# Kernel tuning notes

Hardware: AMD Instinct MI355X
Metric: run time of the kernel (lower is better)

Reference implementation:

```python
import jax, jax.numpy as jnp
import numpy as np

SEQ, D_IN, D_OUT = 8192, 1024, 1024


def setup_inputs() -> dict:
    key = jax.random.key(0)
    kx, kq, kk, kv = jax.random.split(key, 4)
    # torch nn.Linear weights have shape (out_features, in_features)
    s = 1.0 / np.sqrt(D_IN)
    return {
        "x": jax.random.normal(kx, (SEQ, D_IN), dtype=jnp.float32),
        "Wq": jax.random.uniform(kq, (D_OUT, D_IN), dtype=jnp.float32, minval=-s, maxval=s),
        "Wk": jax.random.uniform(kk, (D_OUT, D_IN), dtype=jnp.float32, minval=-s, maxval=s),
        "Wv": jax.random.uniform(kv, (D_OUT, D_IN), dtype=jnp.float32, minval=-s, maxval=s),
    }


def reference(x, Wq, Wk, Wv):
    # Linear (no bias): y = x @ W.T
    q = x @ Wq.T          # [S, D_OUT]
    k = x @ Wk.T          # [S, D_OUT]
    v = x @ Wv.T          # [S, D_OUT]
    scale = 1.0 / jnp.sqrt(jnp.asarray(k.shape[-1], dtype=x.dtype))
    scores = (q @ k.T) * scale            # [S, S]
    weights = jax.nn.softmax(scores, axis=-1)
    return weights @ v                    # [S, D_OUT]
```

## Files before the change

### kernel.cpp

```cpp
#include <hip/hip_runtime.h>
#include <hip/hip_bf16.h>
#include <stdint.h>


#define SEQ 8192
#define DMODEL 1024
#define LOG2E 1.44269504088896340736f
#define GROUP_M 8

typedef __bf16 bf16_t;
typedef __bf16 bf16x8 __attribute__((ext_vector_type(8)));
typedef float f32x4 __attribute__((ext_vector_type(4)));

__global__ __launch_bounds__(256)
void convert_f32_bf16(const float* __restrict__ in, bf16_t* __restrict__ out, long n) {
    long i = ((long)blockIdx.x * 256 + threadIdx.x) * 4;
    if (i + 3 < n) {
        const float4 v = *(const float4*)(in + i);
        union { ushort4 u; bf16_t b[4]; } p;
        p.b[0] = (bf16_t)v.x; p.b[1] = (bf16_t)v.y;
        p.b[2] = (bf16_t)v.z; p.b[3] = (bf16_t)v.w;
        *(ushort4*)(out + i) = p.u;
    }
}

__global__ __launch_bounds__(256)
void add_f32(float* __restrict__ out, const float* __restrict__ part, long n) {
    long i = ((long)blockIdx.x * 256 + threadIdx.x) * 4;
    if (i + 3 < n) {
        float4 a = *(const float4*)(out + i);
        const float4 b = *(const float4*)(part + i);
        a.x += b.x; a.y += b.y; a.z += b.z; a.w += b.w;
        *(float4*)(out + i) = a;
    }
}

__global__ __launch_bounds__(256)
void zero_f32(float* __restrict__ p, int n) {
    int i = blockIdx.x * 256 + threadIdx.x;
    if (i < n) p[i] = 0.0f;
}

template <typename OutT, int MODE>
__global__ __launch_bounds__(512, 2)
void gemm_nt(const bf16_t* __restrict__ A, const bf16_t* __restrict__ B,
             OutT* __restrict__ C0, OutT* __restrict__ C1,
             float* __restrict__ lsum,
             int M, int N, int Kps, int lda, int ldb, int ldc,
             long plane, int cshift, float alpha)
{
    __shared__ bf16_t As[2][256 * 64];
    __shared__ bf16_t Bs[2][256 * 64];

    const int tid  = threadIdx.x;
    const int wave = tid >> 6;
    const int lane = tid & 63;

    const int nbm = M >> 8, nbn = N >> 8;
    const int tiles = nbm * nbn;
    int bid = blockIdx.x;
    const int sid = bid / tiles;
    bid -= sid * tiles;
    const long kbase = (long)sid * Kps;
    OutT* __restrict__ C = sid ? C1 : C0;

    const int per_group = GROUP_M * nbn;
    const int gid   = bid / per_group;
    const int rem   = bid - gid * per_group;
    const int first = gid * GROUP_M;
    const int gsz   = min(nbm - first, GROUP_M);
    const int bm    = first + rem % gsz;
    const int bn    = rem / gsz;
    const long row0 = (long)bm * 256;
    const long col0 = (long)bn * 256;

    const int wm = (wave >> 2) * 128;
    const int wn = (wave & 3) * 64;
    const int lr = lane & 15;
    const int lq = lane >> 4;

    const int rt = tid >> 3;
    const int sl = ((tid & 7) + rt) & 7;
    const bf16_t* pa = A + (row0 + rt) * (long)lda + kbase + sl * 8;
    const bf16_t* pb = B + (col0 + rt) * (long)ldb + kbase + sl * 8;

    const int p0  = (lq - lr) & 7;
    const int p1  = p0 ^ 4;
    const int oA0 = (wm + lr) * 64 + p0 * 8;
    const int oA1 = (wm + lr) * 64 + p1 * 8;
    const int oB0 = (wn + lr) * 64 + p0 * 8;
    const int oB1 = (wn + lr) * 64 + p1 * 8;

    const int nt = Kps >> 6;

    f32x4 acc[8][4] = {};

#define STG_A(kt, bsel, i0)                                                     \
    {                                                                           \
        _Pragma("unroll")                                                       \
        for (int ii = 0; ii < 2; ++ii) {                                        \
            const int i = (i0) + ii;                                            \
            const bf16_t* ga = pa + (long)(kt) * 64 + (long)i * 64 * lda;       \
            __builtin_amdgcn_global_load_lds(                                   \
                (const __attribute__((address_space(1))) uint32_t*)ga,          \
                (__attribute__((address_space(3))) uint32_t*)(As[bsel] + i * 4096 + tid * 8), \
                16, 0, 0);                                                      \
        }                                                                       \
    }
#define STG_B(kt, bsel, i0)                                                     \
    {                                                                           \
        _Pragma("unroll")                                                       \
        for (int ii = 0; ii < 2; ++ii) {                                        \
            const int i = (i0) + ii;                                            \
            const bf16_t* gb = pb + (long)(kt) * 64 + (long)i * 64 * ldb;       \
            __builtin_amdgcn_global_load_lds(                                   \
                (const __attribute__((address_space(1))) uint32_t*)gb,          \
                (__attribute__((address_space(3))) uint32_t*)(Bs[bsel] + i * 4096 + tid * 8), \
                16, 0, 0);                                                      \
        }                                                                       \
    }

    STG_A(0, 0, 0); STG_A(0, 0, 2); STG_B(0, 0, 0); STG_B(0, 0, 2);
    if (nt > 1) STG_A(1, 1, 0);
    asm volatile("s_waitcnt vmcnt(2)" ::: "memory");
    __builtin_amdgcn_s_barrier();

    for (int t = 0; t < nt; ++t) {
        const int c = t & 1;
        const bf16_t* as = As[c];
        const bf16_t* bs = Bs[c];
        const int s1 = (t + 1 < nt);
        const int s2 = (t + 2 < nt);

        bf16x8 a0k0[4], a0k1[4], a1k0[4], a1k1[4];
        bf16x8 b0k0[2], b0k1[2], b1k0[2], b1k1[2];

        #pragma unroll
        for (int mi = 0; mi < 4; ++mi) {
            a0k0[mi] = *(const bf16x8*)(as + oA0 + mi * 1024);
            a0k1[mi] = *(const bf16x8*)(as + oA1 + mi * 1024);
        }
        #pragma unroll
        for (int ni = 0; ni < 2; ++ni) {
            b0k0[ni] = *(const bf16x8*)(bs + oB0 + ni * 1024);
            b0k1[ni] = *(const bf16x8*)(bs + oB1 + ni * 1024);
        }
        if (s1) STG_A(t + 1, c ^ 1, 2);
        asm volatile("s_waitcnt lgkmcnt(8)" ::: "memory");
        __builtin_amdgcn_s_barrier();
        asm volatile("s_waitcnt lgkmcnt(0)" ::: "memory");
        __builtin_amdgcn_s_setprio(1);
        #pragma unroll
        for (int mi = 0; mi < 4; ++mi)
            #pragma unroll
            for (int ni = 0; ni < 2; ++ni)
                acc[mi][ni] = __builtin_amdgcn_mfma_f32_16x16x32_bf16(
                    a0k0[mi], b0k0[ni], acc[mi][ni], 0, 0, 0);
        #pragma unroll
        for (int mi = 0; mi < 4; ++mi)
            #pragma unroll
            for (int ni = 0; ni < 2; ++ni)
                acc[mi][ni] = __builtin_amdgcn_mfma_f32_16x16x32_bf16(
                    a0k1[mi], b0k1[ni], acc[mi][ni], 0, 0, 0);
        __builtin_amdgcn_s_setprio(0);
        __builtin_amdgcn_s_barrier();

        #pragma unroll
        for (int ni = 0; ni < 2; ++ni) {
            b1k0[ni] = *(const bf16x8*)(bs + oB0 + (ni + 2) * 1024);
            b1k1[ni] = *(const bf16x8*)(bs + oB1 + (ni + 2) * 1024);
        }
        if (s1) STG_B(t + 1, c ^ 1, 0);
        __builtin_amdgcn_s_barrier();
        asm volatile("s_waitcnt lgkmcnt(0)" ::: "memory");
        __builtin_amdgcn_s_setprio(1);
        #pragma unroll
        for (int mi = 0; mi < 4; ++mi)
            #pragma unroll
            for (int ni = 0; ni < 2; ++ni)
                acc[mi][ni + 2] = __builtin_amdgcn_mfma_f32_16x16x32_bf16(
                    a0k0[mi], b1k0[ni], acc[mi][ni + 2], 0, 0, 0);
        #pragma unroll
        for (int mi = 0; mi < 4; ++mi)
            #pragma unroll
            for (int ni = 0; ni < 2; ++ni)
                acc[mi][ni + 2] = __builtin_amdgcn_mfma_f32_16x16x32_bf16(
                    a0k1[mi], b1k1[ni], acc[mi][ni + 2], 0, 0, 0);
        __builtin_amdgcn_s_setprio(0);
        __builtin_amdgcn_s_barrier();

        #pragma unroll
        for (int mi = 0; mi < 4; ++mi) {
            a1k0[mi] = *(const bf16x8*)(as + oA0 + (mi + 4) * 1024);
            a1k1[mi] = *(const bf16x8*)(as + oA1 + (mi + 4) * 1024);
        }
        if (s1) STG_B(t + 1, c ^ 1, 2);
        __builtin_amdgcn_s_barrier();
        asm volatile("s_waitcnt lgkmcnt(0)" ::: "memory");
        __builtin_amdgcn_s_setprio(1);
        #pragma unroll
        for (int mi = 0; mi < 4; ++mi)
            #pragma unroll
            for (int ni = 0; ni < 2; ++ni)
                acc[mi + 4][ni] = __builtin_amdgcn_mfma_f32_16x16x32_bf16(
                    a1k0[mi], b0k0[ni], acc[mi + 4][ni], 0, 0, 0);
        #pragma unroll
        for (int mi = 0; mi < 4; ++mi)
            #pragma unroll
            for (int ni = 0; ni < 2; ++ni)
                acc[mi + 4][ni] = __builtin_amdgcn_mfma_f32_16x16x32_bf16(
                    a1k1[mi], b0k1[ni], acc[mi + 4][ni], 0, 0, 0);
        __builtin_amdgcn_s_setprio(0);
        __builtin_amdgcn_s_barrier();

        if (s2) STG_A(t + 2, c, 0);
        asm volatile("s_waitcnt vmcnt(2)" ::: "memory");
        __builtin_amdgcn_s_barrier();
        __builtin_amdgcn_s_setprio(1);
        #pragma unroll
        for (int mi = 0; mi < 4; ++mi)
            #pragma unroll
            for (int ni = 0; ni < 2; ++ni)
                acc[mi + 4][ni + 2] = __builtin_amdgcn_mfma_f32_16x16x32_bf16(
                    a1k0[mi], b1k0[ni], acc[mi + 4][ni + 2], 0, 0, 0);
        #pragma unroll
        for (int mi = 0; mi < 4; ++mi)
            #pragma unroll
            for (int ni = 0; ni < 2; ++ni)
                acc[mi + 4][ni + 2] = __builtin_amdgcn_mfma_f32_16x16x32_bf16(
                    a1k1[mi], b1k1[ni], acc[mi + 4][ni + 2], 0, 0, 0);
        __builtin_amdgcn_s_setprio(0);
        __builtin_amdgcn_s_barrier();
    }
#undef STG_A
#undef STG_B

    OutT* __restrict__ Cb = C + (col0 >> cshift) * plane;
    const int ccol0 = (int)(col0 & (((long)1 << cshift) - 1));

    if (MODE == 1) {
        #pragma unroll
        for (int mi = 0; mi < 8; ++mi)
            #pragma unroll
            for (int rg = 0; rg < 4; ++rg) {
                const long r = row0 + wm + mi * 16 + lq * 4 + rg;
                float part = 0.f;
                #pragma unroll
                for (int ni = 0; ni < 4; ++ni) {
                    const int c = ccol0 + wn + ni * 16 + lr;
                    const float e = exp2f(alpha * acc[mi][ni][rg]);
                    part += e;
                    Cb[r * (long)ldc + c] = (OutT)e;
                }
                part += __shfl_xor(part, 1);
                part += __shfl_xor(part, 2);
                part += __shfl_xor(part, 4);
                part += __shfl_xor(part, 8);
                if (lr == 0) atomicAdd(&lsum[r], part);
            }
    } else if (MODE == 2) {
        #pragma unroll
        for (int mi = 0; mi < 8; ++mi)
            #pragma unroll
            for (int rg = 0; rg < 4; ++rg) {
                const long r = row0 + wm + mi * 16 + lq * 4 + rg;
                const float inv = 1.0f / lsum[r];
                #pragma unroll
                for (int ni = 0; ni < 4; ++ni) {
                    const int c = ccol0 + wn + ni * 16 + lr;
                    Cb[r * (long)ldc + c] = (OutT)(acc[mi][ni][rg] * inv);
                }
            }
    } else {
        #pragma unroll
        for (int mi = 0; mi < 8; ++mi)
            #pragma unroll
            for (int ni = 0; ni < 4; ++ni)
                #pragma unroll
                for (int rg = 0; rg < 4; ++rg) {
                    const long r = row0 + wm + mi * 16 + lq * 4 + rg;
                    const int  c = ccol0 + wn + ni * 16 + lr;
                    Cb[r * (long)ldc + c] = (OutT)(alpha * acc[mi][ni][rg]);
                }
    }
}

__global__ __launch_bounds__(256)
void transpose_bf16(const bf16_t* __restrict__ in, bf16_t* __restrict__ out,
                    int R, int ldin, int ldout)
{
    __shared__ bf16_t tile[32][33];
    const int tx = threadIdx.x & 31;
    const int ty = threadIdx.x >> 5;
    const int c0 = blockIdx.x * 32;
    const int r0 = blockIdx.y * 32;
    #pragma unroll
    for (int j = 0; j < 32; j += 8)
        tile[ty + j][tx] = in[(long)(r0 + ty + j) * ldin + c0 + tx];
    __syncthreads();
    #pragma unroll
    for (int j = 0; j < 32; j += 8)
        out[(long)(c0 + ty + j) * ldout + r0 + tx] = tile[tx][ty + j];
}

extern "C" void kernel_launch(void* const* d_in, const int* in_sizes, int n_in,
                              void* d_out, int out_size, void* d_ws, size_t ws_size,
                              hipStream_t stream)
{
    const float* x  = (const float*)d_in[0];
    const float* Wq = (const float*)d_in[1];
    const float* Wk = (const float*)d_in[2];
    const float* Wv = (const float*)d_in[3];
    float* out = (float*)d_out;

    char* ws = (char*)d_ws;
    const long XN = (long)SEQ * DMODEL;
    const long WN = (long)DMODEL * DMODEL;
    const long SN = (long)SEQ * SEQ;

    bf16_t* xb   = (bf16_t*)ws;
    bf16_t* wcat = (bf16_t*)(ws + XN * 2);
    bf16_t* qb   = (bf16_t*)(ws + XN * 2 + WN * 6);
    bf16_t* kb   = qb + XN;
    bf16_t* vb   = qb + 2 * XN;
    bf16_t* Sb   = (bf16_t*)(ws + XN * 2 + WN * 6 + XN * 6);
    float*  pvp  = (float*)(ws + XN * 2 + WN * 6 + XN * 6 + SN * 2);
    float*  lsum = (float*)(ws + XN * 2 + WN * 6 + XN * 6 + SN * 2 + XN * 4);
    bf16_t* vtb  = xb;

    const size_t base_need = (size_t)(XN * 2 + WN * 6 + XN * 6 + SN * 2);
    const bool use_split = ws_size >= base_need + XN * 4 + SEQ * 4;
    if (!use_split) lsum = (float*)(ws + base_need);

    convert_f32_bf16<<<(int)(XN / 4 / 256), 256, 0, stream>>>(x,  xb, XN);
    convert_f32_bf16<<<(int)(WN / 4 / 256), 256, 0, stream>>>(Wq, wcat,          WN);
    convert_f32_bf16<<<(int)(WN / 4 / 256), 256, 0, stream>>>(Wk, wcat + WN,     WN);
    convert_f32_bf16<<<(int)(WN / 4 / 256), 256, 0, stream>>>(Wv, wcat + 2 * WN, WN);
    zero_f32<<<SEQ / 256, 256, 0, stream>>>(lsum, SEQ);

    dim3 blk256(256);
    dim3 blk512(512);
    gemm_nt<bf16_t, 0><<<(SEQ / 256) * (3 * DMODEL / 256), blk512, 0, stream>>>(
        xb, wcat, qb, qb, nullptr, SEQ, 3 * DMODEL, DMODEL,
        DMODEL, DMODEL, DMODEL, XN, 10, 1.0f);

    transpose_bf16<<<dim3(DMODEL / 32, SEQ / 32), blk256, 0, stream>>>(
        vb, vtb, SEQ, DMODEL, SEQ);

    gemm_nt<bf16_t, 1><<<(SEQ / 256) * (SEQ / 256), blk512, 0, stream>>>(
        qb, kb, Sb, Sb, lsum, SEQ, SEQ, DMODEL,
        DMODEL, DMODEL, SEQ, 0, 30, 0.03125f * LOG2E);

    if (use_split) {
        gemm_nt<float, 2><<<2 * (SEQ / 256) * (DMODEL / 256), blk512, 0, stream>>>(
            Sb, vtb, out, pvp, lsum, SEQ, DMODEL, SEQ / 2,
            SEQ, SEQ, DMODEL, 0, 30, 1.0f);
        add_f32<<<(int)(XN / 4 / 256), 256, 0, stream>>>(out, pvp, XN);
    } else {
        gemm_nt<float, 2><<<(SEQ / 256) * (DMODEL / 256), blk512, 0, stream>>>(
            Sb, vtb, out, out, lsum, SEQ, DMODEL, SEQ,
            SEQ, SEQ, DMODEL, 0, 30, 1.0f);
    }
}
```

Measured before the change: 482.8 us.

## Software-pipeline LDS fragment loads across iterations and cut per-iteration barriers

Restructures the GEMM main loop so the first A/B register fragments for the next K-tile are read from LDS during the current tile's MFMA phases, instead of at the start of each iteration. It also drops most of the per-phase s_barriers in favour of sched_barrier and finer lgkmcnt waits, keeping a single workgroup barrier per iteration around the global-to-LDS staging. The aim is to hide LDS read latency behind MFMAs and reduce synchronisation stalls. In exchange it raises register pressure, and the looser barrier scheme risks LDS races on buffers that are still being overwritten.

Measured after the change: 528.2 us. 9.4% more time.

```diff
diff --git a/kernel.cpp b/kernel.cpp
--- a/kernel.cpp
+++ b/kernel.cpp
@@ -121,34 +121,46 @@
     }
 
     STG_A(0, 0, 0); STG_A(0, 0, 2); STG_B(0, 0, 0); STG_B(0, 0, 2);
-    if (nt > 1) STG_A(1, 1, 0);
-    asm volatile("s_waitcnt vmcnt(2)" ::: "memory");
+    if (nt > 1) {
+        STG_A(1, 1, 0);
+        asm volatile("s_waitcnt vmcnt(2)" ::: "memory");
+    } else {
+        asm volatile("s_waitcnt vmcnt(0)" ::: "memory");
+    }
     __builtin_amdgcn_s_barrier();
+
+    bf16x8 a0k0[4], a0k1[4], a1k0[4], a1k1[4];
+    bf16x8 b0k0[2], b0k1[2], b1k0[2], b1k1[2];
+
+    #pragma unroll
+    for (int mi = 0; mi < 4; ++mi) {
+        a0k0[mi] = *(const bf16x8*)(As[0] + oA0 + mi * 1024);
+        a0k1[mi] = *(const bf16x8*)(As[0] + oA1 + mi * 1024);
+    }
+    #pragma unroll
+    for (int ni = 0; ni < 2; ++ni) {
+        b0k0[ni] = *(const bf16x8*)(Bs[0] + oB0 + ni * 1024);
+        b0k1[ni] = *(const bf16x8*)(Bs[0] + oB1 + ni * 1024);
+    }
 
     for (int t = 0; t < nt; ++t) {
         const int c = t & 1;
-        const bf16_t* as = As[c];
-        const bf16_t* bs = Bs[c];
+        const bf16_t* as  = As[c];
+        const bf16_t* bs  = Bs[c];
+        const bf16_t* asn = As[c ^ 1];
+        const bf16_t* bsn = Bs[c ^ 1];
         const int s1 = (t + 1 < nt);
         const int s2 = (t + 2 < nt);
 
-        bf16x8 a0k0[4], a0k1[4], a1k0[4], a1k1[4];
-        bf16x8 b0k0[2], b0k1[2], b1k0[2], b1k1[2];
-
-        #pragma unroll
-        for (int mi = 0; mi < 4; ++mi) {
-            a0k0[mi] = *(const bf16x8*)(as + oA0 + mi * 1024);
-            a0k1[mi] = *(const bf16x8*)(as + oA1 + mi * 1024);
-        }
+        if (s1) { STG_A(t + 1, c ^ 1, 2); STG_B(t + 1, c ^ 1, 0); }
         #pragma unroll
         for (int ni = 0; ni < 2; ++ni) {
-            b0k0[ni] = *(const bf16x8*)(bs + oB0 + ni * 1024);
-            b0k1[ni] = *(const bf16x8*)(bs + oB1 + ni * 1024);
-        }
-        if (s1) STG_A(t + 1, c ^ 1, 2);
-        asm volatile("s_waitcnt lgkmcnt(8)" ::: "memory");
-        __builtin_amdgcn_s_barrier();
-        asm volatile("s_waitcnt lgkmcnt(0)" ::: "memory");
+            b1k0[ni] = *(const bf16x8*)(bs + oB0 + (ni + 2) * 1024);
+            b1k1[ni] = *(const bf16x8*)(bs + oB1 + (ni + 2) * 1024);
+        }
+
+        asm volatile("s_waitcnt lgkmcnt(4)" ::: "memory");
+        __builtin_amdgcn_sched_barrier(0);
         __builtin_amdgcn_s_setprio(1);
         #pragma unroll
         for (int mi = 0; mi < 4; ++mi)
@@ -163,16 +175,17 @@
                 acc[mi][ni] = __builtin_amdgcn_mfma_f32_16x16x32_bf16(
                     a0k1[mi], b0k1[ni], acc[mi][ni], 0, 0, 0);
         __builtin_amdgcn_s_setprio(0);
-        __builtin_amdgcn_s_barrier();
-
-        #pragma unroll
-        for (int ni = 0; ni < 2; ++ni) {
-            b1k0[ni] = *(const bf16x8*)(bs + oB0 + (ni + 2) * 1024);
-            b1k1[ni] = *(const bf16x8*)(bs + oB1 + (ni + 2) * 1024);
-        }
-        if (s1) STG_B(t + 1, c ^ 1, 0);
-        __builtin_amdgcn_s_barrier();
-        asm volatile("s_waitcnt lgkmcnt(0)" ::: "memory");
+        __builtin_amdgcn_sched_barrier(0);
+
+        #pragma unroll
+        for (int mi = 0; mi < 4; ++mi) {
+            a1k0[mi] = *(const bf16x8*)(as + oA0 + (mi + 4) * 1024);
+            a1k1[mi] = *(const bf16x8*)(as + oA1 + (mi + 4) * 1024);
+        }
+        if (s1) STG_B(t + 1, c ^ 1, 2);
+
+        asm volatile("s_waitcnt lgkmcnt(8)" ::: "memory");
+        __builtin_amdgcn_sched_barrier(0);
         __builtin_amdgcn_s_setprio(1);
         #pragma unroll
         for (int mi = 0; mi < 4; ++mi)
@@ -187,16 +200,27 @@
                 acc[mi][ni + 2] = __builtin_amdgcn_mfma_f32_16x16x32_bf16(
                     a0k1[mi], b1k1[ni], acc[mi][ni + 2], 0, 0, 0);
         __builtin_amdgcn_s_setprio(0);
+        __builtin_amdgcn_sched_barrier(0);
+
+        asm volatile("s_waitcnt lgkmcnt(0)" ::: "memory");
         __builtin_amdgcn_s_barrier();
-
-        #pragma unroll
-        for (int mi = 0; mi < 4; ++mi) {
-            a1k0[mi] = *(const bf16x8*)(as + oA0 + (mi + 4) * 1024);
-            a1k1[mi] = *(const bf16x8*)(as + oA1 + (mi + 4) * 1024);
-        }
-        if (s1) STG_B(t + 1, c ^ 1, 2);
+        if (s2) {
+            STG_A(t + 2, c, 0);
+            asm volatile("s_waitcnt vmcnt(2)" ::: "memory");
+        } else {
+            asm volatile("s_waitcnt vmcnt(0)" ::: "memory");
+        }
         __builtin_amdgcn_s_barrier();
-        asm volatile("s_waitcnt lgkmcnt(0)" ::: "memory");
+
+        if (s1) {
+            #pragma unroll
+            for (int mi = 0; mi < 4; ++mi) {
+                a0k0[mi] = *(const bf16x8*)(asn + oA0 + mi * 1024);
+                a0k1[mi] = *(const bf16x8*)(asn + oA1 + mi * 1024);
+            }
+        }
+        __builtin_amdgcn_sched_barrier(0);
+
         __builtin_amdgcn_s_setprio(1);
         #pragma unroll
         for (int mi = 0; mi < 4; ++mi)
@@ -211,11 +235,17 @@
                 acc[mi + 4][ni] = __builtin_amdgcn_mfma_f32_16x16x32_bf16(
                     a1k1[mi], b0k1[ni], acc[mi + 4][ni], 0, 0, 0);
         __builtin_amdgcn_s_setprio(0);
-        __builtin_amdgcn_s_barrier();
-
-        if (s2) STG_A(t + 2, c, 0);
-        asm volatile("s_waitcnt vmcnt(2)" ::: "memory");
-        __builtin_amdgcn_s_barrier();
+        __builtin_amdgcn_sched_barrier(0);
+
+        if (s1) {
+            #pragma unroll
+            for (int ni = 0; ni < 2; ++ni) {
+                b0k0[ni] = *(const bf16x8*)(bsn + oB0 + ni * 1024);
+                b0k1[ni] = *(const bf16x8*)(bsn + oB1 + ni * 1024);
+            }
+        }
+        __builtin_amdgcn_sched_barrier(0);
+
         __builtin_amdgcn_s_setprio(1);
         #pragma unroll
         for (int mi = 0; mi < 4; ++mi)
@@ -230,7 +260,7 @@
                 acc[mi + 4][ni + 2] = __builtin_amdgcn_mfma_f32_16x16x32_bf16(
                     a1k1[mi], b1k1[ni], acc[mi + 4][ni + 2], 0, 0, 0);
         __builtin_amdgcn_s_setprio(0);
-        __builtin_amdgcn_s_barrier();
+        __builtin_amdgcn_sched_barrier(0);
     }
 #undef STG_A
 #undef STG_B
@@ -247,10 +277,10 @@
                 float part = 0.f;
                 #pragma unroll
                 for (int ni = 0; ni < 4; ++ni) {
-                    const int c = ccol0 + wn + ni * 16 + lr;
+                    const int cc = ccol0 + wn + ni * 16 + lr;
                     const float e = exp2f(alpha * acc[mi][ni][rg]);
                     part += e;
-                    Cb[r * (long)ldc + c] = (OutT)e;
+                    Cb[r * (long)ldc + cc] = (OutT)e;
                 }
                 part += __shfl_xor(part, 1);
                 part += __shfl_xor(part, 2);
@@ -267,8 +297,8 @@
                 const float inv = 1.0f / lsum[r];
                 #pragma unroll
                 for (int ni = 0; ni < 4; ++ni) {
-                    const int c = ccol0 + wn + ni * 16 + lr;
-                    Cb[r * (long)ldc + c] = (OutT)(acc[mi][ni][rg] * inv);
+                    const int cc = ccol0 + wn + ni * 16 + lr;
+                    Cb[r * (long)ldc + cc] = (OutT)(acc[mi][ni][rg] * inv);
                 }
             }
     } else {
@@ -279,8 +309,8 @@
                 #pragma unroll
                 for (int rg = 0; rg < 4; ++rg) {
                     const long r = row0 + wm + mi * 16 + lq * 4 + rg;
-                    const int  c = ccol0 + wn + ni * 16 + lr;
-                    Cb[r * (long)ldc + c] = (OutT)(alpha * acc[mi][ni][rg]);
+                    const int  cc = ccol0 + wn + ni * 16 + lr;
+                    Cb[r * (long)ldc + cc] = (OutT)(alpha * acc[mi][ni][rg]);
                 }
     }
 }
```

## Replace interleaved partial-stage GEMM pipeline with simple double buffering

Applied to the files above, without the earlier changes.

Replaces the fine-grained schedule with plain double buffering in the GEMM main loop. The old loop split each tile's global-to-LDS loads into quarters spread across four MFMA phases, with several barriers per iteration and a stage two tiles ahead. Now each iteration waits for all loads, issues one barrier, then issues the whole next-tile prefetch before the LDS reads and MFMAs. This cuts barrier and waitcnt overhead per K-step, but the load issue is less interleaved with compute and the wait is coarser.

Measured after the change: 512.0 us. 6.0% more time.

```diff
diff --git a/kernel.cpp b/kernel.cpp
--- a/kernel.cpp
+++ b/kernel.cpp
@@ -95,23 +95,18 @@
 
     f32x4 acc[8][4] = {};
 
-#define STG_A(kt, bsel, i0)                                                     \
+#define STG8(kt, bsel)                                                          \
     {                                                                           \
         _Pragma("unroll")                                                       \
-        for (int ii = 0; ii < 2; ++ii) {                                        \
-            const int i = (i0) + ii;                                            \
+        for (int i = 0; i < 4; ++i) {                                           \
             const bf16_t* ga = pa + (long)(kt) * 64 + (long)i * 64 * lda;       \
             __builtin_amdgcn_global_load_lds(                                   \
                 (const __attribute__((address_space(1))) uint32_t*)ga,          \
                 (__attribute__((address_space(3))) uint32_t*)(As[bsel] + i * 4096 + tid * 8), \
                 16, 0, 0);                                                      \
         }                                                                       \
-    }
-#define STG_B(kt, bsel, i0)                                                     \
-    {                                                                           \
         _Pragma("unroll")                                                       \
-        for (int ii = 0; ii < 2; ++ii) {                                        \
-            const int i = (i0) + ii;                                            \
+        for (int i = 0; i < 4; ++i) {                                           \
             const bf16_t* gb = pb + (long)(kt) * 64 + (long)i * 64 * ldb;       \
             __builtin_amdgcn_global_load_lds(                                   \
                 (const __attribute__((address_space(1))) uint32_t*)gb,          \
@@ -120,21 +115,20 @@
         }                                                                       \
     }
 
-    STG_A(0, 0, 0); STG_A(0, 0, 2); STG_B(0, 0, 0); STG_B(0, 0, 2);
-    if (nt > 1) STG_A(1, 1, 0);
-    asm volatile("s_waitcnt vmcnt(2)" ::: "memory");
-    __builtin_amdgcn_s_barrier();
+    STG8(0, 0);
 
     for (int t = 0; t < nt; ++t) {
         const int c = t & 1;
         const bf16_t* as = As[c];
         const bf16_t* bs = Bs[c];
-        const int s1 = (t + 1 < nt);
-        const int s2 = (t + 2 < nt);
-
-        bf16x8 a0k0[4], a0k1[4], a1k0[4], a1k1[4];
-        bf16x8 b0k0[2], b0k1[2], b1k0[2], b1k1[2];
-
+
+        asm volatile("s_waitcnt vmcnt(0)" ::: "memory");
+        __builtin_amdgcn_s_barrier();
+        asm volatile("" ::: "memory");
+
+        if (t + 1 < nt) STG8(t + 1, c ^ 1);
+
+        bf16x8 a0k0[4], a0k1[4], b0k0[2], b0k1[2], b1k0[2], b1k1[2];
         #pragma unroll
         for (int mi = 0; mi < 4; ++mi) {
             a0k0[mi] = *(const bf16x8*)(as + oA0 + mi * 1024);
@@ -144,36 +138,24 @@
         for (int ni = 0; ni < 2; ++ni) {
             b0k0[ni] = *(const bf16x8*)(bs + oB0 + ni * 1024);
             b0k1[ni] = *(const bf16x8*)(bs + oB1 + ni * 1024);
-        }
-        if (s1) STG_A(t + 1, c ^ 1, 2);
-        asm volatile("s_waitcnt lgkmcnt(8)" ::: "memory");
-        __builtin_amdgcn_s_barrier();
-        asm volatile("s_waitcnt lgkmcnt(0)" ::: "memory");
-        __builtin_amdgcn_s_setprio(1);
-        #pragma unroll
-        for (int mi = 0; mi < 4; ++mi)
-            #pragma unroll
-            for (int ni = 0; ni < 2; ++ni)
-                acc[mi][ni] = __builtin_amdgcn_mfma_f32_16x16x32_bf16(
-                    a0k0[mi], b0k0[ni], acc[mi][ni], 0, 0, 0);
-        #pragma unroll
-        for (int mi = 0; mi < 4; ++mi)
-            #pragma unroll
-            for (int ni = 0; ni < 2; ++ni)
-                acc[mi][ni] = __builtin_amdgcn_mfma_f32_16x16x32_bf16(
-                    a0k1[mi], b0k1[ni], acc[mi][ni], 0, 0, 0);
-        __builtin_amdgcn_s_setprio(0);
-        __builtin_amdgcn_s_barrier();
-
-        #pragma unroll
-        for (int ni = 0; ni < 2; ++ni) {
             b1k0[ni] = *(const bf16x8*)(bs + oB0 + (ni + 2) * 1024);
             b1k1[ni] = *(const bf16x8*)(bs + oB1 + (ni + 2) * 1024);
         }
-        if (s1) STG_B(t + 1, c ^ 1, 0);
-        __builtin_amdgcn_s_barrier();
-        asm volatile("s_waitcnt lgkmcnt(0)" ::: "memory");
+
         __builtin_amdgcn_s_setprio(1);
+        #pragma unroll
+        for (int mi = 0; mi < 4; ++mi)
+            #pragma unroll
+            for (int ni = 0; ni < 2; ++ni)
+                acc[mi][ni] = __builtin_amdgcn_mfma_f32_16x16x32_bf16(
+                    a0k0[mi], b0k0[ni], acc[mi][ni], 0, 0, 0);
+        #pragma unroll
+        for (int mi = 0; mi < 4; ++mi)
+            #pragma unroll
+            for (int ni = 0; ni < 2; ++ni)
+                acc[mi][ni] = __builtin_amdgcn_mfma_f32_16x16x32_bf16(
+                    a0k1[mi], b0k1[ni], acc[mi][ni], 0, 0, 0);
+
         #pragma unroll
         for (int mi = 0; mi < 4; ++mi)
             #pragma unroll
@@ -187,16 +169,14 @@
                 acc[mi][ni + 2] = __builtin_amdgcn_mfma_f32_16x16x32_bf16(
                     a0k1[mi], b1k1[ni], acc[mi][ni + 2], 0, 0, 0);
         __builtin_amdgcn_s_setprio(0);
-        __builtin_amdgcn_s_barrier();
-
+
+        bf16x8 a1k0[4], a1k1[4];
         #pragma unroll
         for (int mi = 0; mi < 4; ++mi) {
             a1k0[mi] = *(const bf16x8*)(as + oA0 + (mi + 4) * 1024);
             a1k1[mi] = *(const bf16x8*)(as + oA1 + (mi + 4) * 1024);
         }
-        if (s1) STG_B(t + 1, c ^ 1, 2);
-        __builtin_amdgcn_s_barrier();
-        asm volatile("s_waitcnt lgkmcnt(0)" ::: "memory");
+
         __builtin_amdgcn_s_setprio(1);
         #pragma unroll
         for (int mi = 0; mi < 4; ++mi)
@@ -210,13 +190,7 @@
             for (int ni = 0; ni < 2; ++ni)
                 acc[mi + 4][ni] = __builtin_amdgcn_mfma_f32_16x16x32_bf16(
                     a1k1[mi], b0k1[ni], acc[mi + 4][ni], 0, 0, 0);
-        __builtin_amdgcn_s_setprio(0);
-        __builtin_amdgcn_s_barrier();
-
-        if (s2) STG_A(t + 2, c, 0);
-        asm volatile("s_waitcnt vmcnt(2)" ::: "memory");
-        __builtin_amdgcn_s_barrier();
-        __builtin_amdgcn_s_setprio(1);
+
         #pragma unroll
         for (int mi = 0; mi < 4; ++mi)
             #pragma unroll
@@ -230,10 +204,8 @@
                 acc[mi + 4][ni + 2] = __builtin_amdgcn_mfma_f32_16x16x32_bf16(
                     a1k1[mi], b1k1[ni], acc[mi + 4][ni + 2], 0, 0, 0);
         __builtin_amdgcn_s_setprio(0);
-        __builtin_amdgcn_s_barrier();
-    }
-#undef STG_A
-#undef STG_B
+    }
+#undef STG8
 
     OutT* __restrict__ Cb = C + (col0 >> cshift) * plane;
     const int ccol0 = (int)(col0 & (((long)1 << cshift) - 1));
@@ -247,10 +219,10 @@
                 float part = 0.f;
                 #pragma unroll
                 for (int ni = 0; ni < 4; ++ni) {
-                    const int c = ccol0 + wn + ni * 16 + lr;
+                    const int cc = ccol0 + wn + ni * 16 + lr;
                     const float e = exp2f(alpha * acc[mi][ni][rg]);
                     part += e;
-                    Cb[r * (long)ldc + c] = (OutT)e;
+                    Cb[r * (long)ldc + cc] = (OutT)e;
                 }
                 part += __shfl_xor(part, 1);
                 part += __shfl_xor(part, 2);
@@ -267,8 +239,8 @@
                 const float inv = 1.0f / lsum[r];
                 #pragma unroll
                 for (int ni = 0; ni < 4; ++ni) {
-                    const int c = ccol0 + wn + ni * 16 + lr;
-                    Cb[r * (long)ldc + c] = (OutT)(acc[mi][ni][rg] * inv);
+                    const int cc = ccol0 + wn + ni * 16 + lr;
+                    Cb[r * (long)ldc + cc] = (OutT)(acc[mi][ni][rg] * inv);
                 }
             }
     } else {
@@ -279,8 +251,8 @@
                 #pragma unroll
                 for (int rg = 0; rg < 4; ++rg) {
                     const long r = row0 + wm + mi * 16 + lq * 4 + rg;
-                    const int  c = ccol0 + wn + ni * 16 + lr;
-                    Cb[r * (long)ldc + c] = (OutT)(alpha * acc[mi][ni][rg]);
+                    const int  cc = ccol0 + wn + ni * 16 + lr;
+                    Cb[r * (long)ldc + cc] = (OutT)(alpha * acc[mi][ni][rg]);
                 }
     }
 }
```
